# Performance work log

Hardware: AMD Instinct MI355X
Metric: run time of the kernel (lower is better)

## Reference

```python
import jax, jax.numpy as jnp
import numpy as np

# module constants (match init_kwargs)
D_MODEL = 1024
N_HEADS = 16
D_K = 64
CHUNK_LEN = 64
EPS = 1e-8

B, C, N, NL = 4, 16, 2, 128  # batch, chunks, neighbors, neighbor_len
S = C * CHUNK_LEN            # seq_len = 1024


def setup_inputs() -> dict:
    key = jax.random.key(0)
    ks = jax.random.split(key, 10)
    s = 0.02
    HD = N_HEADS * D_K
    return {
        "h": jax.random.normal(ks[0], (B, S, D_MODEL), jnp.float32),
        "e": jax.random.normal(ks[1], (B, C, N, NL, D_MODEL), jnp.float32),
        "g_norm": jnp.ones((D_MODEL,), jnp.float32),
        "Wq": jax.random.normal(ks[2], (D_MODEL, HD), jnp.float32) * s,
        "bq": jnp.zeros((HD,), jnp.float32),
        "Wk": jax.random.normal(ks[3], (D_MODEL, HD), jnp.float32) * s,
        "bk": jnp.zeros((HD,), jnp.float32),
        "Wv": jax.random.normal(ks[4], (D_MODEL, HD), jnp.float32) * s,
        "bv": jnp.zeros((HD,), jnp.float32),
        "Wo": jax.random.normal(ks[5], (HD, D_MODEL), jnp.float32) * s,
        "bo": jnp.zeros((D_MODEL,), jnp.float32),
    }


def _rmsnorm(x, g):
    return x * g * jax.lax.rsqrt(jnp.mean(x * x, axis=-1, keepdims=True) + EPS)


def reference(h, e, g_norm, Wq, bq, Wk, bk, Wv, bv, Wo, bo):
    b, seq, d = h.shape
    _, c, n, nl, _ = e.shape
    cl = CHUNK_LEN
    scale = 1.0 / np.sqrt(D_K).astype(np.float32)

    h_res = h
    hn = _rmsnorm(h[:, cl - 1:], g_norm)                 # [b, seq-cl+1, d]
    pad = c * cl - hn.shape[1]
    hn = jnp.pad(hn, ((0, 0), (0, pad), (0, 0)))         # [b, c*cl, d]
    hn = hn.reshape(b, c, cl, d)

    q = (hn @ Wq + bq).reshape(b, c, cl, N_HEADS, D_K)       # bcihd
    k = (e @ Wk + bk).reshape(b, c, n, nl, N_HEADS, D_K)     # bcnjhd
    v = (e @ Wv + bv).reshape(b, c, n, nl, N_HEADS, D_K)

    attn = jnp.einsum('bcihd,bcnjhd->bchinj', q, k) * scale  # [b,c,h,i,n,j]
    attn = jax.nn.softmax(attn.reshape(b, c, N_HEADS, cl, n * nl), axis=-1)
    attn = attn.reshape(b, c, N_HEADS, cl, n, nl)

    o = jnp.einsum('bchinj,bcnjhd->bcihd', attn, v)
    o = o.reshape(b, c * cl, N_HEADS * D_K)
    o = o @ Wo + bo                                          # [b, c*cl, d]
    o = jnp.pad(o, ((0, 0), (cl - 1, 0), (0, 0)))            # shift right by cl-1
    return o[:, :seq] + h_res
```

## Files before the change

kernel.cpp:

```cpp
#include <hip/hip_runtime.h>
#include <stdint.h>

#define DEV __device__ __forceinline__

typedef __attribute__((ext_vector_type(8))) __bf16 bf16x8;
typedef __attribute__((ext_vector_type(4))) float floatx4;

DEV unsigned int f2bf(float f) {
  union { float f; unsigned int i; } x; x.f = f;
  unsigned int r = x.i + 0x7FFFu + ((x.i >> 16) & 1u);
  return r >> 16;
}
DEV void gl2lds16(const unsigned short* g, unsigned short* l) {
  __builtin_amdgcn_global_load_lds(
      (const __attribute__((address_space(1))) unsigned int*)g,
      (__attribute__((address_space(3))) unsigned int*)l, 16, 0, 0);
}
DEV floatx4 zero4() { floatx4 z; z[0]=0.f; z[1]=0.f; z[2]=0.f; z[3]=0.f; return z; }

__global__ void cca_prep_k(const float* __restrict__ W0, const float* __restrict__ W1,
                           const float* __restrict__ W2, const float* __restrict__ W3,
                           unsigned short* __restrict__ D0, unsigned short* __restrict__ D1,
                           unsigned short* __restrict__ D2, unsigned short* __restrict__ D3,
                           const float* __restrict__ e, unsigned short* __restrict__ eb,
                           const float* __restrict__ h, const float* __restrict__ g,
                           unsigned short* __restrict__ hn, float* __restrict__ out) {
  __shared__ float tile[64][65];
  int blk = blockIdx.x;
  int t = threadIdx.x;
  if (blk < 1024) {
    const float* W; unsigned short* Wt;
    switch (blk >> 8) {
      case 0: W = W0; Wt = D0; break;
      case 1: W = W1; Wt = D1; break;
      case 2: W = W2; Wt = D2; break;
      default: W = W3; Wt = D3; break;
    }
    int k0 = (blk & 15) * 64, n0 = ((blk >> 4) & 15) * 64;
    int c = t & 63, r4 = t >> 6;
#pragma unroll
    for (int it = 0; it < 16; ++it) {
      int r = it * 4 + r4;
      tile[r][c] = W[(size_t)(k0 + r) * 1024 + n0 + c];
    }
    __syncthreads();
#pragma unroll
    for (int it = 0; it < 16; ++it) {
      int r = it * 4 + r4;
      Wt[(size_t)(n0 + r) * 1024 + k0 + c] = (unsigned short)f2bf(tile[c][r]);
    }
    return;
  }
  if (blk < 17408) {
    int i = (blk - 1024) * 256 + t;
    float4 v = ((const float4*)e)[i];
    uint2 o;
    o.x = f2bf(v.x) | (f2bf(v.y) << 16);
    o.y = f2bf(v.z) | (f2bf(v.w) << 16);
    ((uint2*)eb)[i] = o;
    return;
  }
  if (blk < 21504) {
    int row = blk - 17408;
    int b = row >> 10, p = row & 1023;
    unsigned short* dst = hn + (size_t)row * 1024;
    if (p >= 961) {
      uint2 z; z.x = 0u; z.y = 0u;
      ((uint2*)dst)[t] = z;
      return;
    }
    const float* src = h + ((size_t)(b << 10) + p + 63) * 1024;
    float4 v = ((const float4*)src)[t];
    float ss = v.x*v.x + v.y*v.y + v.z*v.z + v.w*v.w;
#pragma unroll
    for (int m = 32; m > 0; m >>= 1) ss += __shfl_down(ss, m);
    __shared__ float wsum[4];
    int lane = t & 63, wv = t >> 6;
    if (lane == 0) wsum[wv] = ss;
    __syncthreads();
    float tot = wsum[0] + wsum[1] + wsum[2] + wsum[3];
    float r = rsqrtf(tot * (1.0f / 1024.0f) + 1e-8f);
    float4 gv = ((const float4*)g)[t];
    uint2 outp;
    outp.x = f2bf(v.x * gv.x * r) | (f2bf(v.y * gv.y * r) << 16);
    outp.y = f2bf(v.z * gv.z * r) | (f2bf(v.w * gv.w * r) << 16);
    ((uint2*)dst)[t] = outp;
    return;
  }
  {
    int idx = (blk - 21504) * 256 + t;
    const int n4 = 4 * 63 * 1024 / 4;
    if (idx < n4) {
      int e4 = idx * 4;
      int b = e4 / (63 * 1024);
      int r = e4 - b * (63 * 1024);
      size_t off = (size_t)b * 1024 * 1024 + (size_t)r;
      *(float4*)(out + off) = *(const float4*)(h + off);
    }
  }
}

__launch_bounds__(256, 2)
__global__ void cca_gemmQKV_k(const unsigned short* __restrict__ eb,
                              const unsigned short* __restrict__ WkvT,
                              const float* __restrict__ bk,
                              const float* __restrict__ bv,
                              unsigned short* __restrict__ KVb,
                              const unsigned short* __restrict__ hn,
                              const unsigned short* __restrict__ WqT,
                              const float* __restrict__ bq,
                              unsigned short* __restrict__ Qb) {
  __shared__ unsigned short Ash[128 * 64];
  __shared__ unsigned short Bsh[128 * 64];
  int blk = blockIdx.x;
  const unsigned short *A, *Bt; const float *b1, *b2; unsigned short* C;
  int N, tM, tN;
  if (blk < 2048) {
    A = eb; Bt = WkvT; b1 = bk; b2 = bv; C = KVb; N = 2048;
    tM = (blk & 127) * 128; tN = (blk >> 7) * 128;
  } else {
    int q = blk - 2048;
    A = hn; Bt = WqT; b1 = bq; b2 = nullptr; C = Qb; N = 1024;
    tM = (q & 31) * 128; tN = (q >> 5) * 128;
  }
  int t = threadIdx.x, lane = t & 63, wv = t >> 6;
  int wm = wv >> 1, wn = wv & 1;
  int l15 = lane & 15, quad = lane >> 4;
  int arow = lane >> 3, achk = lane & 7;
  int gchk = achk ^ arow;
  floatx4 acc[4][4];
#pragma unroll
  for (int i = 0; i < 4; ++i)
#pragma unroll
    for (int j = 0; j < 4; ++j) acc[i][j] = zero4();

  for (int k0 = 0; k0 < 1024; k0 += 64) {
    __syncthreads();
#pragma unroll
    for (int ii = 0; ii < 4; ++ii) {
      int seg = ii * 4 + wv;
      int row = seg * 8 + arow;
      gl2lds16(A + (size_t)(tM + row) * 1024 + k0 + gchk * 8, Ash + seg * 512);
      gl2lds16(Bt + (size_t)(tN + row) * 1024 + k0 + gchk * 8, Bsh + seg * 512);
    }
    __syncthreads();
#pragma unroll
    for (int h = 0; h < 2; ++h) {
      int u = (h << 2) | quad;
      bf16x8 af[4], bfv[4];
#pragma unroll
      for (int mt = 0; mt < 4; ++mt) {
        int r = wm * 64 + mt * 16 + l15;
        af[mt] = *(const bf16x8*)&Ash[r * 64 + ((u ^ (l15 & 7)) << 3)];
      }
#pragma unroll
      for (int nt = 0; nt < 4; ++nt) {
        int r = wn * 64 + nt * 16 + l15;
        bfv[nt] = *(const bf16x8*)&Bsh[r * 64 + ((u ^ (l15 & 7)) << 3)];
      }
#pragma unroll
      for (int mt = 0; mt < 4; ++mt)
#pragma unroll
        for (int nt = 0; nt < 4; ++nt)
          acc[mt][nt] = __builtin_amdgcn_mfma_f32_16x16x32_bf16(af[mt], bfv[nt], acc[mt][nt], 0, 0, 0);
    }
  }

#pragma unroll
  for (int mt = 0; mt < 4; ++mt) {
    int mrow = tM + wm * 64 + mt * 16 + quad * 4;
#pragma unroll
    for (int nt = 0; nt < 4; ++nt) {
      int ncol = tN + wn * 64 + nt * 16 + l15;
      float bs = (b2 != nullptr && ncol >= 1024) ? b2[ncol - 1024] : b1[ncol];
#pragma unroll
      for (int r = 0; r < 4; ++r) {
        int m = mrow + r;
        C[(size_t)m * N + ncol] = (unsigned short)f2bf(acc[mt][nt][r] + bs);
      }
    }
  }
}

__launch_bounds__(256, 2)
__global__ void cca_gemmO_k(const unsigned short* __restrict__ A,
                            const unsigned short* __restrict__ Bt,
                            const float* __restrict__ bias,
                            const float* __restrict__ resid,
                            float* __restrict__ out) {
  __shared__ unsigned short Ash[128 * 64];
  __shared__ unsigned short Bsh[64 * 64];
  int tM = blockIdx.x * 128, tN = blockIdx.y * 64;
  int t = threadIdx.x, lane = t & 63, wv = t >> 6;
  int wm = wv >> 1, wn = wv & 1;
  int l15 = lane & 15, quad = lane >> 4;
  int arow = lane >> 3, achk = lane & 7;
  int gchk = achk ^ arow;
  floatx4 acc[4][2];
#pragma unroll
  for (int i = 0; i < 4; ++i)
#pragma unroll
    for (int j = 0; j < 2; ++j) acc[i][j] = zero4();

  for (int k0 = 0; k0 < 1024; k0 += 64) {
    __syncthreads();
#pragma unroll
    for (int ii = 0; ii < 4; ++ii) {
      int seg = ii * 4 + wv;
      int row = seg * 8 + arow;
      gl2lds16(A + (size_t)(tM + row) * 1024 + k0 + gchk * 8, Ash + seg * 512);
    }
#pragma unroll
    for (int ii = 0; ii < 2; ++ii) {
      int seg = ii * 4 + wv;
      int row = seg * 8 + arow;
      gl2lds16(Bt + (size_t)(tN + row) * 1024 + k0 + gchk * 8, Bsh + seg * 512);
    }
    __syncthreads();
#pragma unroll
    for (int h = 0; h < 2; ++h) {
      int u = (h << 2) | quad;
      bf16x8 af[4], bfv[2];
#pragma unroll
      for (int mt = 0; mt < 4; ++mt) {
        int r = wm * 64 + mt * 16 + l15;
        af[mt] = *(const bf16x8*)&Ash[r * 64 + ((u ^ (l15 & 7)) << 3)];
      }
#pragma unroll
      for (int nt = 0; nt < 2; ++nt) {
        int r = wn * 32 + nt * 16 + l15;
        bfv[nt] = *(const bf16x8*)&Bsh[r * 64 + ((u ^ (l15 & 7)) << 3)];
      }
#pragma unroll
      for (int mt = 0; mt < 4; ++mt)
#pragma unroll
        for (int nt = 0; nt < 2; ++nt)
          acc[mt][nt] = __builtin_amdgcn_mfma_f32_16x16x32_bf16(af[mt], bfv[nt], acc[mt][nt], 0, 0, 0);
    }
  }

#pragma unroll
  for (int mt = 0; mt < 4; ++mt) {
    int mrow = tM + wm * 64 + mt * 16 + quad * 4;
#pragma unroll
    for (int nt = 0; nt < 2; ++nt) {
      int ncol = tN + wn * 32 + nt * 16 + l15;
      float bs = bias[ncol];
#pragma unroll
      for (int r = 0; r < 4; ++r) {
        int m = mrow + r;
        int p = m & 1023;
        if (p < 961) {
          size_t o = (size_t)(m + 63) * 1024 + (size_t)ncol;
          out[o] = acc[mt][nt][r] + bs + resid[o];
        }
      }
    }
  }
}

__global__ void cca_vt_k(const unsigned short* __restrict__ KV,
                         unsigned short* __restrict__ VTb) {
  __shared__ unsigned short tile[256 * 66];
  int bch = blockIdx.x;
  int hh = bch & 15, c = (bch >> 4) & 15, b = bch >> 8;
  size_t kvbase = (size_t)b * 4096 + (size_t)c * 256;
  int t = threadIdx.x;
#pragma unroll
  for (int it = 0; it < 16; ++it) {
    int flat = it * 256 + t;
    int row = flat >> 4, cu = flat & 15;
    uint2 v = *(const uint2*)(KV + (kvbase + row) * 2048 + 1024 + hh * 64 + cu * 4);
    int d0 = cu * 4;
    tile[row * 66 + d0 + 0] = (unsigned short)(v.x & 0xffff);
    tile[row * 66 + d0 + 1] = (unsigned short)(v.x >> 16);
    tile[row * 66 + d0 + 2] = (unsigned short)(v.y & 0xffff);
    tile[row * 66 + d0 + 3] = (unsigned short)(v.y >> 16);
  }
  __syncthreads();
  unsigned short* dst = VTb + (size_t)bch * 16384;
#pragma unroll
  for (int it = 0; it < 16; ++it) {
    int flat = it * 256 + t;
    int d = flat >> 6, ju = flat & 63;
    int j = ju * 4;
    unsigned int lo = (unsigned int)tile[(j + 0) * 66 + d] |
                      ((unsigned int)tile[(j + 1) * 66 + d] << 16);
    unsigned int hi = (unsigned int)tile[(j + 2) * 66 + d] |
                      ((unsigned int)tile[(j + 3) * 66 + d] << 16);
    int u = j >> 3, joff = j & 7;
    int phys = d * 256 + ((u ^ (d & 7)) << 3) + joff;
    uint2 o; o.x = lo; o.y = hi;
    *(uint2*)(dst + phys) = o;
  }
}

__launch_bounds__(256, 2)
__global__ void cca_attn_k(const unsigned short* __restrict__ Q,
                           const unsigned short* __restrict__ KV,
                           const unsigned short* __restrict__ VTb,
                           unsigned short* __restrict__ O) {
  __shared__ unsigned short smemA[64 * 64 + 256 * 64];
  __shared__ unsigned short VTlds[64 * 256];
  unsigned short* Qsh = smemA;
  unsigned short* Ksh = smemA + 64 * 64;
  unsigned short* Psh = smemA;
  int bch = blockIdx.x;
  int hh = bch & 15, c = (bch >> 4) & 15, b = bch >> 8;
  int t = threadIdx.x, lane = t & 63, wv = t >> 6;
  int l15 = lane & 15, quad = lane >> 4;
  size_t qbase = (size_t)b * 1024 + (size_t)c * 64;
  size_t kvbase = (size_t)b * 4096 + (size_t)c * 256;
  int hoff = hh * 64;

  {
    int rowi = lane >> 3, chk = lane & 7;
#pragma unroll
    for (int ii = 0; ii < 2; ++ii) {
      int seg = wv + ii * 4;
      int row = seg * 8 + rowi;
      gl2lds16(Q + (qbase + row) * 1024 + hoff + chk * 8, Qsh + seg * 512);
    }
#pragma unroll
    for (int ii = 0; ii < 8; ++ii) {
      int seg = wv + ii * 4;
      int row = seg * 8 + rowi;
      gl2lds16(KV + (kvbase + row) * 2048 + hoff + chk * 8, Ksh + seg * 512);
    }
    const unsigned short* vsrc = VTb + (size_t)bch * 16384;
#pragma unroll
    for (int ii = 0; ii < 8; ++ii) {
      int seg = wv + ii * 4;
      gl2lds16(vsrc + seg * 512 + lane * 8, VTlds + seg * 512);
    }
  }
  __syncthreads();

  floatx4 st[16];
#pragma unroll
  for (int i = 0; i < 16; ++i) st[i] = zero4();
  bf16x8 a0 = *(const bf16x8*)&Qsh[(wv * 16 + l15) * 64 + quad * 8];
  bf16x8 a1 = *(const bf16x8*)&Qsh[(wv * 16 + l15) * 64 + 32 + quad * 8];
#pragma unroll
  for (int kt = 0; kt < 16; ++kt) {
    bf16x8 b0 = *(const bf16x8*)&Ksh[(kt * 16 + l15) * 64 + quad * 8];
    bf16x8 b1 = *(const bf16x8*)&Ksh[(kt * 16 + l15) * 64 + 32 + quad * 8];
    st[kt] = __builtin_amdgcn_mfma_f32_16x16x32_bf16(a0, b0, st[kt], 0, 0, 0);
    st[kt] = __builtin_amdgcn_mfma_f32_16x16x32_bf16(a1, b1, st[kt], 0, 0, 0);
  }
  __syncthreads();

  const float scale = 0.125f;
#pragma unroll
  for (int r = 0; r < 4; ++r) {
    float mx = -1e30f;
#pragma unroll
    for (int kt = 0; kt < 16; ++kt) mx = fmaxf(mx, st[kt][r]);
    mx = fmaxf(mx, __shfl_xor(mx, 1));
    mx = fmaxf(mx, __shfl_xor(mx, 2));
    mx = fmaxf(mx, __shfl_xor(mx, 4));
    mx = fmaxf(mx, __shfl_xor(mx, 8));
    float sum = 0.f;
#pragma unroll
    for (int kt = 0; kt < 16; ++kt) {
      float e = __expf((st[kt][r] - mx) * scale);
      st[kt][r] = e;
      sum += e;
    }
    sum += __shfl_xor(sum, 1);
    sum += __shfl_xor(sum, 2);
    sum += __shfl_xor(sum, 4);
    sum += __shfl_xor(sum, 8);
    float inv = 1.0f / sum;
    int prow = wv * 16 + quad * 4 + r;
#pragma unroll
    for (int kt = 0; kt < 16; ++kt)
      Psh[prow * 264 + kt * 16 + l15] = (unsigned short)f2bf(st[kt][r] * inv);
  }

  floatx4 ot[4];
#pragma unroll
  for (int nt = 0; nt < 4; ++nt) ot[nt] = zero4();
#pragma unroll
  for (int kt2 = 0; kt2 < 8; ++kt2) {
    bf16x8 ap = *(const bf16x8*)&Psh[(wv * 16 + l15) * 264 + kt2 * 32 + quad * 8];
#pragma unroll
    for (int nt = 0; nt < 4; ++nt) {
      int vrow = nt * 16 + l15;
      int u = kt2 * 4 + quad;
      bf16x8 bv8 = *(const bf16x8*)&VTlds[vrow * 256 + ((u ^ (vrow & 7)) << 3)];
      ot[nt] = __builtin_amdgcn_mfma_f32_16x16x32_bf16(ap, bv8, ot[nt], 0, 0, 0);
    }
  }
#pragma unroll
  for (int nt = 0; nt < 4; ++nt) {
#pragma unroll
    for (int r = 0; r < 4; ++r) {
      int i = wv * 16 + quad * 4 + r;
      int dcol = hoff + nt * 16 + l15;
      O[(qbase + i) * 1024 + dcol] = (unsigned short)f2bf(ot[nt][r]);
    }
  }
}

extern "C" void kernel_launch(void* const* d_in, const int* in_sizes, int n_in,
                              void* d_out, int out_size, void* d_ws, size_t ws_size,
                              hipStream_t stream) {
  const float* h  = (const float*)d_in[0];
  const float* e  = (const float*)d_in[1];
  const float* g  = (const float*)d_in[2];
  const float* Wq = (const float*)d_in[3];
  const float* bq = (const float*)d_in[4];
  const float* Wk = (const float*)d_in[5];
  const float* bk = (const float*)d_in[6];
  const float* Wv = (const float*)d_in[7];
  const float* bv = (const float*)d_in[8];
  const float* Wo = (const float*)d_in[9];
  const float* bo = (const float*)d_in[10];
  float* out = (float*)d_out;

  unsigned short* ws   = (unsigned short*)d_ws;
  unsigned short* hn   = ws;
  unsigned short* WqT  = hn   + (size_t)4096 * 1024;
  unsigned short* WkvT = WqT  + (size_t)1024 * 1024;
  unsigned short* WoT  = WkvT + (size_t)2048 * 1024;
  unsigned short* Qb   = WoT  + (size_t)1024 * 1024;
  unsigned short* KVb  = Qb   + (size_t)4096 * 1024;
  unsigned short* Ob   = KVb  + (size_t)16384 * 2048;
  unsigned short* eb   = Ob   + (size_t)4096 * 1024;
  unsigned short* VTb  = eb;

  cca_prep_k<<<21756, 256, 0, stream>>>(
      Wq, Wk, Wv, Wo, WqT, WkvT, WkvT + (size_t)1024 * 1024, WoT,
      e, eb, h, g, hn, out);

  cca_gemmQKV_k<<<2304, 256, 0, stream>>>(eb, WkvT, bk, bv, KVb,
                                          hn, WqT, bq, Qb);

  cca_vt_k<<<1024, 256, 0, stream>>>(KVb, VTb);

  cca_attn_k<<<1024, 256, 0, stream>>>(Qb, KVb, VTb, Ob);

  cca_gemmO_k<<<dim3(32, 16), 256, 0, stream>>>(Ob, WoT, bo, h, out);
}
```

Measured before the change: 275.1 us.

## Fuse V transpose into QKV GEMM epilogue and drop separate transpose kernel

The QKV GEMM epilogue now writes V tiles directly in the swizzled transposed layout the attention kernel expects, stored in the V half of the KV buffer. This removes the separate cca_vt_k launch along with its extra read and write of V through global memory. Block index mapping also changes so that consecutive blocks share an M tile and iterate over N tiles, which may improve L2 reuse of A. The cost is scattered 8-byte stores in the V epilogue and a less contiguous V load pattern in attention.

```diff
diff --git a/kernel.cpp b/kernel.cpp
--- a/kernel.cpp
+++ b/kernel.cpp
@@ -113,15 +113,17 @@
   __shared__ unsigned short Ash[128 * 64];
   __shared__ unsigned short Bsh[128 * 64];
   int blk = blockIdx.x;
-  const unsigned short *A, *Bt; const float *b1, *b2; unsigned short* C;
-  int N, tM, tN;
-  if (blk < 2048) {
-    A = eb; Bt = WkvT; b1 = bk; b2 = bv; C = KVb; N = 2048;
-    tM = (blk & 127) * 128; tN = (blk >> 7) * 128;
+  const unsigned short *A, *Bt;
+  int tM, tN;
+  bool isQ = (blk >= 2048), isV = false;
+  if (!isQ) {
+    int mblk = blk >> 4, n = blk & 15;
+    tM = mblk * 128; tN = n * 128; isV = (n >= 8);
+    A = eb; Bt = WkvT;
   } else {
     int q = blk - 2048;
-    A = hn; Bt = WqT; b1 = bq; b2 = nullptr; C = Qb; N = 1024;
-    tM = (q & 31) * 128; tN = (q >> 5) * 128;
+    tM = (q >> 3) * 128; tN = (q & 7) * 128;
+    A = hn; Bt = WqT;
   }
   int t = threadIdx.x, lane = t & 63, wv = t >> 6;
   int wm = wv >> 1, wn = wv & 1;
@@ -145,8 +147,8 @@
     }
     __syncthreads();
 #pragma unroll
-    for (int h = 0; h < 2; ++h) {
-      int u = (h << 2) | quad;
+    for (int hseg = 0; hseg < 2; ++hseg) {
+      int u = (hseg << 2) | quad;
       bf16x8 af[4], bfv[4];
 #pragma unroll
       for (int mt = 0; mt < 4; ++mt) {
@@ -166,17 +168,40 @@
     }
   }
 
+  if (isV) {
+    int chunk = tM >> 8;
+    int keybase = tM & 255;
+    unsigned short* vdst = KVb + (size_t)chunk * 524288 + 1024;
+#pragma unroll
+    for (int mt = 0; mt < 4; ++mt) {
+      int key = keybase + wm * 64 + mt * 16 + quad * 4;
+      int u = key >> 3, j0 = key & 7;
+#pragma unroll
+      for (int nt = 0; nt < 4; ++nt) {
+        int dcol = (tN - 1024) + wn * 64 + nt * 16 + l15;
+        int hh = dcol >> 6, d = dcol & 63;
+        float bs = bv[dcol];
+        uint2 o;
+        o.x = f2bf(acc[mt][nt][0] + bs) | (f2bf(acc[mt][nt][1] + bs) << 16);
+        o.y = f2bf(acc[mt][nt][2] + bs) | (f2bf(acc[mt][nt][3] + bs) << 16);
+        int idx = d * 256 + ((u ^ (d & 7)) << 3) + j0;
+        *(uint2*)(vdst + (size_t)(hh * 16 + (idx >> 10)) * 2048 + (idx & 1023)) = o;
+      }
+    }
+    return;
+  }
 #pragma unroll
   for (int mt = 0; mt < 4; ++mt) {
     int mrow = tM + wm * 64 + mt * 16 + quad * 4;
 #pragma unroll
     for (int nt = 0; nt < 4; ++nt) {
       int ncol = tN + wn * 64 + nt * 16 + l15;
-      float bs = (b2 != nullptr && ncol >= 1024) ? b2[ncol - 1024] : b1[ncol];
+      float bs = isQ ? bq[ncol] : bk[ncol];
 #pragma unroll
       for (int r = 0; r < 4; ++r) {
         int m = mrow + r;
-        C[(size_t)m * N + ncol] = (unsigned short)f2bf(acc[mt][nt][r] + bs);
+        if (isQ) Qb[(size_t)m * 1024 + ncol] = (unsigned short)f2bf(acc[mt][nt][r] + bs);
+        else     KVb[(size_t)m * 2048 + ncol] = (unsigned short)f2bf(acc[mt][nt][r] + bs);
       }
     }
   }
@@ -218,8 +243,8 @@
     }
     __syncthreads();
 #pragma unroll
-    for (int h = 0; h < 2; ++h) {
-      int u = (h << 2) | quad;
+    for (int hseg = 0; hseg < 2; ++hseg) {
+      int u = (hseg << 2) | quad;
       bf16x8 af[4], bfv[2];
 #pragma unroll
       for (int mt = 0; mt < 4; ++mt) {
@@ -259,46 +284,9 @@
   }
 }
 
-__global__ void cca_vt_k(const unsigned short* __restrict__ KV,
-                         unsigned short* __restrict__ VTb) {
-  __shared__ unsigned short tile[256 * 66];
-  int bch = blockIdx.x;
-  int hh = bch & 15, c = (bch >> 4) & 15, b = bch >> 8;
-  size_t kvbase = (size_t)b * 4096 + (size_t)c * 256;
-  int t = threadIdx.x;
-#pragma unroll
-  for (int it = 0; it < 16; ++it) {
-    int flat = it * 256 + t;
-    int row = flat >> 4, cu = flat & 15;
-    uint2 v = *(const uint2*)(KV + (kvbase + row) * 2048 + 1024 + hh * 64 + cu * 4);
-    int d0 = cu * 4;
-    tile[row * 66 + d0 + 0] = (unsigned short)(v.x & 0xffff);
-    tile[row * 66 + d0 + 1] = (unsigned short)(v.x >> 16);
-    tile[row * 66 + d0 + 2] = (unsigned short)(v.y & 0xffff);
-    tile[row * 66 + d0 + 3] = (unsigned short)(v.y >> 16);
-  }
-  __syncthreads();
-  unsigned short* dst = VTb + (size_t)bch * 16384;
-#pragma unroll
-  for (int it = 0; it < 16; ++it) {
-    int flat = it * 256 + t;
-    int d = flat >> 6, ju = flat & 63;
-    int j = ju * 4;
-    unsigned int lo = (unsigned int)tile[(j + 0) * 66 + d] |
-                      ((unsigned int)tile[(j + 1) * 66 + d] << 16);
-    unsigned int hi = (unsigned int)tile[(j + 2) * 66 + d] |
-                      ((unsigned int)tile[(j + 3) * 66 + d] << 16);
-    int u = j >> 3, joff = j & 7;
-    int phys = d * 256 + ((u ^ (d & 7)) << 3) + joff;
-    uint2 o; o.x = lo; o.y = hi;
-    *(uint2*)(dst + phys) = o;
-  }
-}
-
 __launch_bounds__(256, 2)
 __global__ void cca_attn_k(const unsigned short* __restrict__ Q,
                            const unsigned short* __restrict__ KV,
-                           const unsigned short* __restrict__ VTb,
                            unsigned short* __restrict__ O) {
   __shared__ unsigned short smemA[64 * 64 + 256 * 64];
   __shared__ unsigned short VTlds[64 * 256];
@@ -327,11 +315,13 @@
       int row = seg * 8 + rowi;
       gl2lds16(KV + (kvbase + row) * 2048 + hoff + chk * 8, Ksh + seg * 512);
     }
-    const unsigned short* vsrc = VTb + (size_t)bch * 16384;
+    const unsigned short* vbase = KV + (size_t)(b * 16 + c) * 524288 + 1024;
 #pragma unroll
     for (int ii = 0; ii < 8; ++ii) {
       int seg = wv + ii * 4;
-      gl2lds16(vsrc + seg * 512 + lane * 8, VTlds + seg * 512);
+      int i = seg * 512 + lane * 8;
+      gl2lds16(vbase + (size_t)(hh * 16 + (i >> 10)) * 2048 + (i & 1023),
+               VTlds + seg * 512);
     }
   }
   __syncthreads();
@@ -428,7 +418,6 @@
   unsigned short* KVb  = Qb   + (size_t)4096 * 1024;
   unsigned short* Ob   = KVb  + (size_t)16384 * 2048;
   unsigned short* eb   = Ob   + (size_t)4096 * 1024;
-  unsigned short* VTb  = eb;
 
   cca_prep_k<<<21756, 256, 0, stream>>>(
       Wq, Wk, Wv, Wo, WqT, WkvT, WkvT + (size_t)1024 * 1024, WoT,
@@ -437,9 +426,7 @@
   cca_gemmQKV_k<<<2304, 256, 0, stream>>>(eb, WkvT, bk, bv, KVb,
                                           hn, WqT, bq, Qb);
 
-  cca_vt_k<<<1024, 256, 0, stream>>>(KVb, VTb);
-
-  cca_attn_k<<<1024, 256, 0, stream>>>(Qb, KVb, VTb, Ob);
+  cca_attn_k<<<1024, 256, 0, stream>>>(Qb, KVb, Ob);
 
   cca_gemmO_k<<<dim3(32, 16), 256, 0, stream>>>(Ob, WoT, bo, h, out);
 }
```

Result: slower. 281.0 us (+2.1%).
